# Performance work log

Measured on AMD Instinct MI355X. Metric: run time of the kernel, lower is better.

The kernel has to match this reference:

```python
import jax, jax.numpy as jnp
import numpy as np

D_MODEL = 384; NHEAD = 8; HEAD_DIM = D_MODEL // NHEAD
NPTS = 4; LENC = 6; LDEC = 6; DFFN = 1536
BS = 2; SD = 12; SH = 12; SW = 12; NQ = 300
S = SD * SH * SW
_SCALE = 0.02
MSDA_KEYS = ('off_w', 'off_b', 'aw_w', 'aw_b', 'vp_w', 'vp_b', 'op_w', 'op_b')


def _ln(x, g, b, eps=1e-5):
    m = x.mean(-1, keepdims=True)
    v = ((x - m) ** 2).mean(-1, keepdims=True)
    return (x - m) / jnp.sqrt(v + eps) * g + b


def _lin(x, w, b):
    return x @ w.T + b


def _trilinear(val, loc):
    # val [B,C,D,H,W]; loc [B,Q,3] normalized (x,y,z) in [0,1].
    # align_corners=False grid_sample semantics, zero padding outside.
    B, C, Dd, Hh, Ww = val.shape
    x = loc[..., 0] * Ww - 0.5
    y = loc[..., 1] * Hh - 0.5
    z = loc[..., 2] * Dd - 0.5
    x0, y0, z0 = jnp.floor(x), jnp.floor(y), jnp.floor(z)
    fx, fy, fz = x - x0, y - y0, z - z0
    bidx = jnp.arange(B)[:, None]
    out = jnp.zeros((B, loc.shape[1], C), val.dtype)
    for dz in (0, 1):
        zi = z0 + dz
        wz = fz if dz else 1.0 - fz
        for dy in (0, 1):
            yi = y0 + dy
            wy = fy if dy else 1.0 - fy
            for dx in (0, 1):
                xi = x0 + dx
                wx = fx if dx else 1.0 - fx
                inb = (xi >= 0) & (xi < Ww) & (yi >= 0) & (yi < Hh) & (zi >= 0) & (zi < Dd)
                v = val[bidx, :,
                        jnp.clip(zi, 0, Dd - 1).astype(jnp.int32),
                        jnp.clip(yi, 0, Hh - 1).astype(jnp.int32),
                        jnp.clip(xi, 0, Ww - 1).astype(jnp.int32)]  # [B,Q,C]
                out = out + (wz * wy * wx * inb)[..., None] * v
    return out


def _msda(query, ref, src, pad_mask, p):
    # 3D multi-scale deformable attention, single feature level.
    B, Lq, _ = query.shape
    value = _lin(src, p['vp_w'], p['vp_b'])
    value = jnp.where(pad_mask[..., None], 0.0, value).reshape(B, S, NHEAD, HEAD_DIM)
    off = _lin(query, p['off_w'], p['off_b']).reshape(B, Lq, NHEAD, NPTS, 3)
    aw = jax.nn.softmax(_lin(query, p['aw_w'], p['aw_b']).reshape(B, Lq, NHEAD, NPTS), -1)
    norm = jnp.array([SW, SH, SD], jnp.float32)  # (x,y,z) normalizer
    loc = ref[:, :, None, None, :] + off / norm  # [B,Lq,H,P,3]
    val = value.transpose(0, 2, 3, 1).reshape(B * NHEAD, HEAD_DIM, SD, SH, SW)
    locf = loc.transpose(0, 2, 1, 3, 4).reshape(B * NHEAD, Lq * NPTS, 3)
    samp = _trilinear(val, locf).reshape(B, NHEAD, Lq, NPTS, HEAD_DIM)
    out = jnp.einsum('bqhp,bhqpc->bqhc', aw, samp).reshape(B, Lq, D_MODEL)
    return _lin(out, p['op_w'], p['op_b'])


def _mha(q, k, v, in_w, in_b, out_w, out_b):
    B, L, d = q.shape
    qp = _lin(q, in_w[:d], in_b[:d]).reshape(B, L, NHEAD, HEAD_DIM)
    kp = _lin(k, in_w[d:2 * d], in_b[d:2 * d]).reshape(B, L, NHEAD, HEAD_DIM)
    vp = _lin(v, in_w[2 * d:], in_b[2 * d:]).reshape(B, L, NHEAD, HEAD_DIM)
    attn = jax.nn.softmax(jnp.einsum('bqhc,bkhc->bhqk', qp, kp) * (1.0 / float(np.sqrt(HEAD_DIM))), -1)
    o = jnp.einsum('bhqk,bkhc->bqhc', attn, vp).reshape(B, L, d)
    return _lin(o, out_w, out_b)


def _forward(a):
    src = a['srcs'].reshape(BS, D_MODEL, S).transpose(0, 2, 1)
    pos = a['pos_embeds'].reshape(BS, D_MODEL, S).transpose(0, 2, 1) + a['level_embed'][0]
    mask = a['masks'].reshape(BS, S)
    m = a['masks']
    valid = jnp.stack([(~m[:, 0, 0, :]).sum(1) / SW,
                       (~m[:, 0, :, 0]).sum(1) / SH,
                       (~m[:, :, 0, 0]).sum(1) / SD], -1).astype(jnp.float32)  # [B,3] (w,h,d)
    rz, ry, rx = jnp.meshgrid((jnp.arange(SD, dtype=jnp.float32) + 0.5) / SD,
                              (jnp.arange(SH, dtype=jnp.float32) + 0.5) / SH,
                              (jnp.arange(SW, dtype=jnp.float32) + 0.5) / SW, indexing='ij')
    enc_ref = jnp.stack([rx.ravel(), ry.ravel(), rz.ravel()], -1)[None] * valid[:, None]  # [B,S,3]
    x = src
    for l in range(LENC):
        p = {n: a['e_' + n][l] for n in MSDA_KEYS}
        x2 = _msda(x + pos, enc_ref, x, mask, p)
        x = _ln(x + x2, a['e_n1_g'][l], a['e_n1_b'][l])
        h = jax.nn.relu(_lin(x, a['e_l1_w'][l], a['e_l1_b'][l]))
        x = _ln(x + _lin(h, a['e_l2_w'][l], a['e_l2_b'][l]), a['e_n2_g'][l], a['e_n2_b'][l])
    memory = x
    qe = jnp.broadcast_to(a['query_embed'][None, :, :D_MODEL], (BS, NQ, D_MODEL))
    y = jnp.broadcast_to(a['query_embed'][None, :, D_MODEL:], (BS, NQ, D_MODEL))
    ref_pts = jax.nn.sigmoid(_lin(qe, a['ref_w'], a['ref_b']))  # [B,NQ,3]
    dec_ref = ref_pts * valid[:, None]  # reference_points * valid_ratios (single level)
    for l in range(LDEC):
        q = y + qe
        y2 = _mha(q, q, y, a['d_sa_in_w'][l], a['d_sa_in_b'][l], a['d_sa_out_w'][l], a['d_sa_out_b'][l])
        y = _ln(y + y2, a['d_n2_g'][l], a['d_n2_b'][l])
        p = {n: a['d_' + n][l] for n in MSDA_KEYS}
        y2 = _msda(y + qe, dec_ref, memory, mask, p)
        y = _ln(y + y2, a['d_n1_g'][l], a['d_n1_b'][l])
        h = jax.nn.relu(_lin(y, a['d_l1_w'][l], a['d_l1_b'][l]))
        y = _ln(y + _lin(h, a['d_l2_w'][l], a['d_l2_b'][l]), a['d_n3_g'][l], a['d_n3_b'][l])
    return y


def setup_inputs():
    ks = iter(jax.random.split(jax.random.key(0), 40))

    def w(*shape):
        return jax.random.normal(next(ks), shape, jnp.float32) * _SCALE

    z = lambda *s: jnp.zeros(s, jnp.float32)
    o = lambda *s: jnp.ones(s, jnp.float32)
    inp = {
        'srcs': jax.random.normal(next(ks), (BS, D_MODEL, SD, SH, SW), jnp.float32),
        'masks': jnp.zeros((BS, SD, SH, SW), bool),
        'query_embed': jax.random.normal(next(ks), (NQ, 2 * D_MODEL), jnp.float32),
        'pos_embeds': jax.random.normal(next(ks), (BS, D_MODEL, SD, SH, SW), jnp.float32),
        'level_embed': jax.random.normal(next(ks), (1, D_MODEL), jnp.float32),
        'ref_w': w(3, D_MODEL), 'ref_b': z(3),
    }
    for pre, L in (('e_', LENC), ('d_', LDEC)):
        inp[pre + 'off_w'] = w(L, NHEAD * NPTS * 3, D_MODEL); inp[pre + 'off_b'] = z(L, NHEAD * NPTS * 3)
        inp[pre + 'aw_w'] = w(L, NHEAD * NPTS, D_MODEL); inp[pre + 'aw_b'] = z(L, NHEAD * NPTS)
        inp[pre + 'vp_w'] = w(L, D_MODEL, D_MODEL); inp[pre + 'vp_b'] = z(L, D_MODEL)
        inp[pre + 'op_w'] = w(L, D_MODEL, D_MODEL); inp[pre + 'op_b'] = z(L, D_MODEL)
        inp[pre + 'n1_g'] = o(L, D_MODEL); inp[pre + 'n1_b'] = z(L, D_MODEL)
        inp[pre + 'l1_w'] = w(L, DFFN, D_MODEL); inp[pre + 'l1_b'] = z(L, DFFN)
        inp[pre + 'l2_w'] = w(L, D_MODEL, DFFN); inp[pre + 'l2_b'] = z(L, D_MODEL)
        inp[pre + 'n2_g'] = o(L, D_MODEL); inp[pre + 'n2_b'] = z(L, D_MODEL)
    inp['d_sa_in_w'] = w(LDEC, 3 * D_MODEL, D_MODEL); inp['d_sa_in_b'] = z(LDEC, 3 * D_MODEL)
    inp['d_sa_out_w'] = w(LDEC, D_MODEL, D_MODEL); inp['d_sa_out_b'] = z(LDEC, D_MODEL)
    inp['d_n3_g'] = o(LDEC, D_MODEL); inp['d_n3_b'] = z(LDEC, D_MODEL)
    return inp


def reference(srcs, masks, query_embed, pos_embeds, level_embed, ref_w, ref_b,
              e_off_w, e_off_b, e_aw_w, e_aw_b, e_vp_w, e_vp_b, e_op_w, e_op_b,
              e_n1_g, e_n1_b, e_l1_w, e_l1_b, e_l2_w, e_l2_b, e_n2_g, e_n2_b,
              d_off_w, d_off_b, d_aw_w, d_aw_b, d_vp_w, d_vp_b, d_op_w, d_op_b,
              d_n1_g, d_n1_b, d_sa_in_w, d_sa_in_b, d_sa_out_w, d_sa_out_b,
              d_n2_g, d_n2_b, d_l1_w, d_l1_b, d_l2_w, d_l2_b, d_n3_g, d_n3_b):
    return _forward(dict(locals()))
```

## Files before the change

kernel.cpp:

```cpp
#include <hip/hip_runtime.h>
#include <math.h>

#define BS_   2
#define S_    1728
#define C_    384
#define H_    8
#define HD_   48
#define DFFN_ 1536
#define NQ_   300
#define GD_   12

typedef __attribute__((ext_vector_type(8))) short short8;
typedef __attribute__((ext_vector_type(4))) float f32x4;

__device__ __forceinline__ ushort f2bf(float f) {
    union { float f; uint u; } v; v.f = f;
    uint u = v.u;
    uint r = (u + 0x7FFFu + ((u >> 16) & 1u)) >> 16;
    return (ushort)r;
}

__global__ __launch_bounds__(256) void f2bf_kernel(
    const float* __restrict__ src, ushort* __restrict__ dst, int n2)
{
    int i = blockIdx.x * 256 + threadIdx.x;
    if (i < n2) {
        float2 v = ((const float2*)src)[i];
        ushort2 o; o.x = f2bf(v.x); o.y = f2bf(v.y);
        ((ushort2*)dst)[i] = o;
    }
}

__global__ __launch_bounds__(256) void gemm_bf16_kernel(
    const ushort* __restrict__ A, const ushort* __restrict__ W,
    const float* __restrict__ bias, void* __restrict__ Co,
    int M, int N, int K, int flags)
{
    __shared__ __align__(16) ushort As[64][40];
    __shared__ __align__(16) ushort Ws[64][40];

    const int tid  = threadIdx.x;
    const int m0 = blockIdx.y * 64;
    const int n0 = blockIdx.x * 64;

    const int srow = tid >> 2;
    const int sch  = tid & 3;
    const int gmA  = m0 + srow;
    const int gnW  = n0 + srow;
    const size_t aBase = (size_t)gmA * K + sch * 8;
    const size_t wBase = (size_t)gnW * K + sch * 8;

    const int lane = tid & 63;
    const int w    = tid >> 6;
    const int wr   = (w >> 1) * 32;
    const int wc   = (w & 1) * 32;
    const int fr   = lane & 15;
    const int fks  = (lane >> 4) * 8;

    f32x4 acc[2][2] = {};

    short8 va = {}, vw = {};
    if (gmA < M) va = *(const short8*)(A + aBase);
    if (gnW < N) vw = *(const short8*)(W + wBase);

    for (int k0 = 0; k0 < K; k0 += 32) {
        *(short8*)&As[srow][sch * 8] = va;
        *(short8*)&Ws[srow][sch * 8] = vw;
        __syncthreads();
        if (k0 + 32 < K) {
            va = (gmA < M) ? *(const short8*)(A + aBase + k0 + 32) : short8{};
            vw = (gnW < N) ? *(const short8*)(W + wBase + k0 + 32) : short8{};
        }
        short8 af[2], bf[2];
        #pragma unroll
        for (int mi = 0; mi < 2; ++mi)
            af[mi] = *(const short8*)&As[wr + mi * 16 + fr][fks];
        #pragma unroll
        for (int ni = 0; ni < 2; ++ni)
            bf[ni] = *(const short8*)&Ws[wc + ni * 16 + fr][fks];
        #pragma unroll
        for (int mi = 0; mi < 2; ++mi)
            #pragma unroll
            for (int ni = 0; ni < 2; ++ni)
                acc[mi][ni] = __builtin_amdgcn_mfma_f32_16x16x32_bf16(
                    af[mi], bf[ni], acc[mi][ni], 0, 0, 0);
        __syncthreads();
    }

    const int r0 = (lane >> 4) * 4;
    const int relu = flags & 1;
    const int obf  = flags & 2;
    float* Cf = (float*)Co;
    ushort* Ch = (ushort*)Co;
    #pragma unroll
    for (int mi = 0; mi < 2; ++mi) {
        #pragma unroll
        for (int ni = 0; ni < 2; ++ni) {
            int gn = n0 + wc + ni * 16 + fr;
            if (gn >= N) continue;
            float bv = bias[gn];
            #pragma unroll
            for (int j = 0; j < 4; ++j) {
                int gm = m0 + wr + mi * 16 + r0 + j;
                if (gm >= M) continue;
                float v = acc[mi][ni][j] + bv;
                if (relu) v = fmaxf(v, 0.f);
                if (obf) Ch[(size_t)gm * N + gn] = f2bf(v);
                else     Cf[(size_t)gm * N + gn] = v;
            }
        }
    }
}

__global__ __launch_bounds__(64) void ln_kernel(
    const float* __restrict__ res, const float* __restrict__ delta,
    const float* __restrict__ g, const float* __restrict__ b,
    float* __restrict__ out, ushort* __restrict__ out_bf)
{
    const int row  = blockIdx.x;
    const int lane = threadIdx.x;
    const float* r = res   + (size_t)row * C_;
    const float* d = delta + (size_t)row * C_;
    float vals[6];
    float s = 0.f;
    #pragma unroll
    for (int i = 0; i < 6; ++i) {
        int c = lane + 64 * i;
        vals[i] = r[c] + d[c];
        s += vals[i];
    }
    #pragma unroll
    for (int off = 32; off; off >>= 1) s += __shfl_xor(s, off);
    float mean = s * (1.f / C_);
    float vs = 0.f;
    #pragma unroll
    for (int i = 0; i < 6; ++i) { float t = vals[i] - mean; vs += t * t; }
    #pragma unroll
    for (int off = 32; off; off >>= 1) vs += __shfl_xor(vs, off);
    float rstd = rsqrtf(vs * (1.f / C_) + 1e-5f);
    float* o = out + (size_t)row * C_;
    ushort* ob = out_bf + (size_t)row * C_;
    #pragma unroll
    for (int i = 0; i < 6; ++i) {
        int c = lane + 64 * i;
        float v = (vals[i] - mean) * rstd * g[c] + b[c];
        o[c] = v;
        ob[c] = f2bf(v);
    }
}

__global__ __launch_bounds__(384) void msda_kernel(
    const float* __restrict__ value,
    const float* __restrict__ offr,
    const float* __restrict__ awr,
    const float* __restrict__ ref,
    ushort* __restrict__ out,
    int Lq)
{
    const int bq = blockIdx.x;
    const int b = bq / Lq, q = bq % Lq;
    const int t = threadIdx.x;
    const int h = t / HD_, c = t % HD_;

    const float* aw = awr + ((size_t)(b * Lq + q)) * 32 + h * 4;
    float a0 = aw[0], a1 = aw[1], a2 = aw[2], a3 = aw[3];
    float mx = fmaxf(fmaxf(a0, a1), fmaxf(a2, a3));
    float e0 = __expf(a0 - mx), e1 = __expf(a1 - mx), e2 = __expf(a2 - mx), e3 = __expf(a3 - mx);
    float inv = 1.f / (e0 + e1 + e2 + e3);
    float wgt[4] = { e0 * inv, e1 * inv, e2 * inv, e3 * inv };

    const float* off = offr + ((size_t)(b * Lq + q)) * 96 + h * 12;
    float rx = ref[q * 3 + 0], ry = ref[q * 3 + 1], rz = ref[q * 3 + 2];
    const float* vb = value + (size_t)b * S_ * C_ + h * HD_ + c;

    float acc = 0.f;
    #pragma unroll
    for (int p = 0; p < 4; ++p) {
        float x = (rx + off[p * 3 + 0] * (1.f / GD_)) * GD_ - 0.5f;
        float y = (ry + off[p * 3 + 1] * (1.f / GD_)) * GD_ - 0.5f;
        float z = (rz + off[p * 3 + 2] * (1.f / GD_)) * GD_ - 0.5f;
        float x0f = floorf(x), y0f = floorf(y), z0f = floorf(z);
        float fx = x - x0f, fy = y - y0f, fz = z - z0f;
        int x0 = (int)x0f, y0 = (int)y0f, z0 = (int)z0f;
        float pv = 0.f;
        #pragma unroll
        for (int dz = 0; dz < 2; ++dz) {
            int zi = z0 + dz;
            if (zi < 0 || zi >= GD_) continue;
            float wz = dz ? fz : 1.f - fz;
            #pragma unroll
            for (int dy = 0; dy < 2; ++dy) {
                int yi = y0 + dy;
                if (yi < 0 || yi >= GD_) continue;
                float wy = dy ? fy : 1.f - fy;
                #pragma unroll
                for (int dx = 0; dx < 2; ++dx) {
                    int xi = x0 + dx;
                    if (xi < 0 || xi >= GD_) continue;
                    float wx = dx ? fx : 1.f - fx;
                    int s = (zi * GD_ + yi) * GD_ + xi;
                    pv += wz * wy * wx * vb[(size_t)s * C_];
                }
            }
        }
        acc += wgt[p] * pv;
    }
    out[((size_t)(b * Lq + q)) * C_ + t] = f2bf(acc);
}

__global__ __launch_bounds__(256) void attn_scores_kernel(
    const float* __restrict__ qp, const float* __restrict__ kp, float* __restrict__ sc)
{
    int idx = blockIdx.x * 256 + threadIdx.x;
    const int total = BS_ * H_ * NQ_ * NQ_;
    if (idx >= total) return;
    int j = idx % NQ_; int r = idx / NQ_;
    int i = r % NQ_;   r /= NQ_;
    int h = r % H_;    int b = r / H_;
    const float* qv = qp + ((size_t)(b * NQ_ + i)) * C_ + h * HD_;
    const float* kv = kp + ((size_t)(b * NQ_ + j)) * C_ + h * HD_;
    float s = 0.f;
    #pragma unroll
    for (int c = 0; c < HD_; ++c) s = fmaf(qv[c], kv[c], s);
    sc[idx] = s * 0.14433756729740643f;
}

__global__ __launch_bounds__(64) void softmax300_kernel(float* __restrict__ sc)
{
    const int row = blockIdx.x;
    float* p = sc + (size_t)row * NQ_;
    const int lane = threadIdx.x;
    float v[5];
    float mx = -INFINITY;
    #pragma unroll
    for (int i = 0; i < 5; ++i) {
        int c = lane + 64 * i;
        v[i] = (c < NQ_) ? p[c] : -INFINITY;
        mx = fmaxf(mx, v[i]);
    }
    #pragma unroll
    for (int off = 32; off; off >>= 1) mx = fmaxf(mx, __shfl_xor(mx, off));
    float s = 0.f;
    #pragma unroll
    for (int i = 0; i < 5; ++i) {
        int c = lane + 64 * i;
        v[i] = (c < NQ_) ? __expf(v[i] - mx) : 0.f;
        s += v[i];
    }
    #pragma unroll
    for (int off = 32; off; off >>= 1) s += __shfl_xor(s, off);
    float inv = 1.f / s;
    #pragma unroll
    for (int i = 0; i < 5; ++i) {
        int c = lane + 64 * i;
        if (c < NQ_) p[c] = v[i] * inv;
    }
}

__global__ __launch_bounds__(256) void attn_out_kernel(
    const float* __restrict__ sc, const float* __restrict__ vp, ushort* __restrict__ o)
{
    int idx = blockIdx.x * 256 + threadIdx.x;
    const int total = BS_ * NQ_ * C_;
    if (idx >= total) return;
    int c = idx % C_; int r = idx / C_;
    int i = r % NQ_;  int b = r / NQ_;
    int h = c / HD_;
    const float* srow = sc + (((size_t)(b * H_ + h)) * NQ_ + i) * NQ_;
    const float* v = vp + (size_t)b * NQ_ * C_ + c;
    float acc = 0.f;
    for (int j = 0; j < NQ_; ++j) acc = fmaf(srow[j], v[(size_t)j * C_], acc);
    o[idx] = f2bf(acc);
}

__global__ __launch_bounds__(256) void prep_kernel(
    const float* __restrict__ srcs, const float* __restrict__ posin,
    const float* __restrict__ lvl, float* __restrict__ x, ushort* __restrict__ x_bf,
    float* __restrict__ pos)
{
    int idx = blockIdx.x * 256 + threadIdx.x;
    const int total = BS_ * S_ * C_;
    if (idx >= total) return;
    int c = idx % C_; int r = idx / C_;
    int s = r % S_;   int b = r / S_;
    size_t si = ((size_t)b * C_ + c) * S_ + s;
    float xv = srcs[si];
    x[idx]   = xv;
    x_bf[idx] = f2bf(xv);
    pos[idx] = posin[si] + lvl[c];
}

__global__ __launch_bounds__(64) void encref_kernel(float* __restrict__ eref)
{
    int s = blockIdx.x * 64 + threadIdx.x;
    if (s >= S_) return;
    int w = s % GD_, h = (s / GD_) % GD_, d = s / (GD_ * GD_);
    eref[s * 3 + 0] = (w + 0.5f) / GD_;
    eref[s * 3 + 1] = (h + 0.5f) / GD_;
    eref[s * 3 + 2] = (d + 0.5f) / GD_;
}

__global__ __launch_bounds__(64) void decref_kernel(
    const float* __restrict__ qemb, const float* __restrict__ rw,
    const float* __restrict__ rb, float* __restrict__ dref)
{
    int idx = blockIdx.x * 64 + threadIdx.x;
    if (idx >= NQ_ * 3) return;
    int d = idx % 3, q = idx / 3;
    const float* qe = qemb + (size_t)q * 768;
    const float* w = rw + d * C_;
    float s = rb[d];
    for (int c = 0; c < C_; ++c) s = fmaf(qe[c], w[c], s);
    dref[idx] = 1.f / (1.f + __expf(-s));
}

__global__ __launch_bounds__(256) void add_bf_kernel(
    const float* __restrict__ a, const float* __restrict__ b, ushort* __restrict__ o, int n)
{
    int idx = blockIdx.x * 256 + threadIdx.x;
    if (idx < n) o[idx] = f2bf(a[idx] + b[idx]);
}

__global__ __launch_bounds__(256) void add_qe_kernel(
    const float* __restrict__ y, const float* __restrict__ qemb, ushort* __restrict__ o)
{
    int idx = blockIdx.x * 256 + threadIdx.x;
    const int total = BS_ * NQ_ * C_;
    if (idx >= total) return;
    int c = idx % C_; int q = (idx / C_) % NQ_;
    o[idx] = f2bf(y[idx] + qemb[(size_t)q * 768 + c]);
}

__global__ __launch_bounds__(256) void init_y_kernel(
    const float* __restrict__ qemb, float* __restrict__ y, ushort* __restrict__ y_bf)
{
    int idx = blockIdx.x * 256 + threadIdx.x;
    const int total = BS_ * NQ_ * C_;
    if (idx >= total) return;
    int c = idx % C_; int q = (idx / C_) % NQ_;
    float v = qemb[(size_t)q * 768 + 384 + c];
    y[idx] = v;
    y_bf[idx] = f2bf(v);
}

static inline void gemm(const ushort* A, const ushort* W, const float* bias, void* C,
                        int M, int N, int K, int flags, hipStream_t s)
{
    dim3 g((N + 63) / 64, (M + 63) / 64);
    hipLaunchKernelGGL(gemm_bf16_kernel, g, dim3(256), 0, s, A, W, bias, C, M, N, K, flags);
}

static inline void conv_w(const float* src, ushort* dst, size_t n, hipStream_t s)
{
    int n2 = (int)(n / 2);
    hipLaunchKernelGGL(f2bf_kernel, dim3((n2 + 255) / 256), dim3(256), 0, s, src, dst, n2);
}

extern "C" void kernel_launch(void* const* d_in, const int* in_sizes, int n_in,
                              void* d_out, int out_size, void* d_ws, size_t ws_size,
                              hipStream_t stream)
{
    const float* srcs    = (const float*)d_in[0];
    const float* qemb    = (const float*)d_in[2];
    const float* posin   = (const float*)d_in[3];
    const float* lvl     = (const float*)d_in[4];
    const float* ref_w   = (const float*)d_in[5];
    const float* ref_b   = (const float*)d_in[6];
    const float* e_off_w = (const float*)d_in[7];
    const float* e_off_b = (const float*)d_in[8];
    const float* e_aw_w  = (const float*)d_in[9];
    const float* e_aw_b  = (const float*)d_in[10];
    const float* e_vp_w  = (const float*)d_in[11];
    const float* e_vp_b  = (const float*)d_in[12];
    const float* e_op_w  = (const float*)d_in[13];
    const float* e_op_b  = (const float*)d_in[14];
    const float* e_n1_g  = (const float*)d_in[15];
    const float* e_n1_b  = (const float*)d_in[16];
    const float* e_l1_w  = (const float*)d_in[17];
    const float* e_l1_b  = (const float*)d_in[18];
    const float* e_l2_w  = (const float*)d_in[19];
    const float* e_l2_b  = (const float*)d_in[20];
    const float* e_n2_g  = (const float*)d_in[21];
    const float* e_n2_b  = (const float*)d_in[22];
    const float* dd_off_w = (const float*)d_in[23];
    const float* dd_off_b = (const float*)d_in[24];
    const float* dd_aw_w  = (const float*)d_in[25];
    const float* dd_aw_b  = (const float*)d_in[26];
    const float* dd_vp_w  = (const float*)d_in[27];
    const float* dd_vp_b  = (const float*)d_in[28];
    const float* dd_op_w  = (const float*)d_in[29];
    const float* dd_op_b  = (const float*)d_in[30];
    const float* dd_n1_g  = (const float*)d_in[31];
    const float* dd_n1_b  = (const float*)d_in[32];
    const float* dd_l1_w  = (const float*)d_in[33];
    const float* dd_l1_b  = (const float*)d_in[34];
    const float* dd_l2_w  = (const float*)d_in[35];
    const float* dd_l2_b  = (const float*)d_in[36];
    const float* dd_n2_g  = (const float*)d_in[37];
    const float* dd_n2_b  = (const float*)d_in[38];
    const float* sa_in_w  = (const float*)d_in[39];
    const float* sa_in_b  = (const float*)d_in[40];
    const float* sa_out_w = (const float*)d_in[41];
    const float* sa_out_b = (const float*)d_in[42];
    const float* dd_n3_g  = (const float*)d_in[43];
    const float* dd_n3_b  = (const float*)d_in[44];

    float* ws = (float*)d_ws;
    size_t o = 0;
    const size_t NXC = (size_t)BS_ * S_ * C_;
    const size_t NYC = (size_t)BS_ * NQ_ * C_;
    float* x     = ws + o; o += NXC;
    float* pos   = ws + o; o += NXC;
    float* value = ws + o; o += NXC;
    float* x2    = ws + o; o += NXC;
    float* offb  = ws + o; o += (size_t)BS_ * S_ * 96;
    float* awb   = ws + o; o += (size_t)BS_ * S_ * 32;
    float* eref  = ws + o; o += (size_t)S_ * 3 + 64;
    float* dref  = ws + o; o += (size_t)NQ_ * 3 + 64;
    float* y     = ws + o; o += NYC;
    float* qp    = ws + o; o += NYC;
    float* kp    = ws + o; o += NYC;
    float* vpb   = ws + o; o += NYC;
    float* sc    = ws + o; o += (size_t)BS_ * H_ * NQ_ * NQ_;
    o = (o + 7) & ~(size_t)7;

    ushort* bws = (ushort*)(ws + o);
    size_t ob = 0;
    ushort* x_bf    = bws + ob; ob += NXC;
    ushort* qb_bf   = bws + ob; ob += NXC;
    ushort* samp_bf = bws + ob; ob += NXC;
    ushort* hbuf_bf = bws + ob; ob += (size_t)BS_ * S_ * DFFN_;
    ushort* y_bf    = bws + ob; ob += NYC;
    const size_t SZ_OFF = (size_t)6 * 96 * C_;
    const size_t SZ_AW  = (size_t)6 * 32 * C_;
    const size_t SZ_SQ  = (size_t)6 * C_ * C_;
    const size_t SZ_L1  = (size_t)6 * DFFN_ * C_;
    ushort* wb_e_off = bws + ob; ob += SZ_OFF;
    ushort* wb_e_aw  = bws + ob; ob += SZ_AW;
    ushort* wb_e_vp  = bws + ob; ob += SZ_SQ;
    ushort* wb_e_op  = bws + ob; ob += SZ_SQ;
    ushort* wb_e_l1  = bws + ob; ob += SZ_L1;
    ushort* wb_e_l2  = bws + ob; ob += SZ_L1;
    ushort* wb_d_off = bws + ob; ob += SZ_OFF;
    ushort* wb_d_aw  = bws + ob; ob += SZ_AW;
    ushort* wb_d_vp  = bws + ob; ob += SZ_SQ;
    ushort* wb_d_op  = bws + ob; ob += SZ_SQ;
    ushort* wb_d_l1  = bws + ob; ob += SZ_L1;
    ushort* wb_d_l2  = bws + ob; ob += SZ_L1;
    ushort* wb_sa_in = bws + ob; ob += (size_t)6 * 3 * C_ * C_;
    ushort* wb_sa_out= bws + ob; ob += SZ_SQ;

    conv_w(e_off_w, wb_e_off, SZ_OFF, stream);
    conv_w(e_aw_w,  wb_e_aw,  SZ_AW,  stream);
    conv_w(e_vp_w,  wb_e_vp,  SZ_SQ,  stream);
    conv_w(e_op_w,  wb_e_op,  SZ_SQ,  stream);
    conv_w(e_l1_w,  wb_e_l1,  SZ_L1,  stream);
    conv_w(e_l2_w,  wb_e_l2,  SZ_L1,  stream);
    conv_w(dd_off_w, wb_d_off, SZ_OFF, stream);
    conv_w(dd_aw_w,  wb_d_aw,  SZ_AW,  stream);
    conv_w(dd_vp_w,  wb_d_vp,  SZ_SQ,  stream);
    conv_w(dd_op_w,  wb_d_op,  SZ_SQ,  stream);
    conv_w(dd_l1_w,  wb_d_l1,  SZ_L1,  stream);
    conv_w(dd_l2_w,  wb_d_l2,  SZ_L1,  stream);
    conv_w(sa_in_w,  wb_sa_in, (size_t)6 * 3 * C_ * C_, stream);
    conv_w(sa_out_w, wb_sa_out, SZ_SQ, stream);

    const int nEnc = BS_ * S_ * C_;
    const int nDec = BS_ * NQ_ * C_;
    const int encBlocks = (nEnc + 255) / 256;
    const int decBlocks = (nDec + 255) / 256;

    hipLaunchKernelGGL(prep_kernel, dim3(encBlocks), dim3(256), 0, stream, srcs, posin, lvl, x, x_bf, pos);
    hipLaunchKernelGGL(encref_kernel, dim3((S_ + 63) / 64), dim3(64), 0, stream, eref);

    for (int l = 0; l < 6; ++l) {
        hipLaunchKernelGGL(add_bf_kernel, dim3(encBlocks), dim3(256), 0, stream, x, pos, qb_bf, nEnc);
        gemm(x_bf, wb_e_vp + (size_t)l * C_ * C_, e_vp_b + (size_t)l * C_, value, BS_ * S_, C_, C_, 0, stream);
        gemm(qb_bf, wb_e_off + (size_t)l * 96 * C_, e_off_b + (size_t)l * 96, offb, BS_ * S_, 96, C_, 0, stream);
        gemm(qb_bf, wb_e_aw + (size_t)l * 32 * C_, e_aw_b + (size_t)l * 32, awb, BS_ * S_, 32, C_, 0, stream);
        hipLaunchKernelGGL(msda_kernel, dim3(BS_ * S_), dim3(384), 0, stream,
                           value, offb, awb, eref, samp_bf, S_);
        gemm(samp_bf, wb_e_op + (size_t)l * C_ * C_, e_op_b + (size_t)l * C_, x2, BS_ * S_, C_, C_, 0, stream);
        hipLaunchKernelGGL(ln_kernel, dim3(BS_ * S_), dim3(64), 0, stream,
                           x, x2, e_n1_g + (size_t)l * C_, e_n1_b + (size_t)l * C_, x, x_bf);
        gemm(x_bf, wb_e_l1 + (size_t)l * DFFN_ * C_, e_l1_b + (size_t)l * DFFN_, hbuf_bf,
             BS_ * S_, DFFN_, C_, 1 | 2, stream);
        gemm(hbuf_bf, wb_e_l2 + (size_t)l * C_ * DFFN_, e_l2_b + (size_t)l * C_, x2,
             BS_ * S_, C_, DFFN_, 0, stream);
        hipLaunchKernelGGL(ln_kernel, dim3(BS_ * S_), dim3(64), 0, stream,
                           x, x2, e_n2_g + (size_t)l * C_, e_n2_b + (size_t)l * C_, x, x_bf);
    }

    hipLaunchKernelGGL(init_y_kernel, dim3(decBlocks), dim3(256), 0, stream, qemb, y, y_bf);
    hipLaunchKernelGGL(decref_kernel, dim3((NQ_ * 3 + 63) / 64), dim3(64), 0, stream,
                       qemb, ref_w, ref_b, dref);

    const int scTotal = BS_ * H_ * NQ_ * NQ_;
    for (int l = 0; l < 6; ++l) {
        const ushort* inw = wb_sa_in + (size_t)l * 3 * C_ * C_;
        const float*  inb = sa_in_b + (size_t)l * 3 * C_;

        hipLaunchKernelGGL(add_qe_kernel, dim3(decBlocks), dim3(256), 0, stream, y, qemb, qb_bf);
        gemm(qb_bf, inw,                       inb,          qp,  BS_ * NQ_, C_, C_, 0, stream);
        gemm(qb_bf, inw + (size_t)C_ * C_,     inb + C_,     kp,  BS_ * NQ_, C_, C_, 0, stream);
        gemm(y_bf,  inw + (size_t)2 * C_ * C_, inb + 2 * C_, vpb, BS_ * NQ_, C_, C_, 0, stream);
        hipLaunchKernelGGL(attn_scores_kernel, dim3((scTotal + 255) / 256), dim3(256), 0, stream,
                           qp, kp, sc);
        hipLaunchKernelGGL(softmax300_kernel, dim3(BS_ * H_ * NQ_), dim3(64), 0, stream, sc);
        hipLaunchKernelGGL(attn_out_kernel, dim3(decBlocks), dim3(256), 0, stream, sc, vpb, samp_bf);
        gemm(samp_bf, wb_sa_out + (size_t)l * C_ * C_, sa_out_b + (size_t)l * C_, x2,
             BS_ * NQ_, C_, C_, 0, stream);
        hipLaunchKernelGGL(ln_kernel, dim3(BS_ * NQ_), dim3(64), 0, stream,
                           y, x2, dd_n2_g + (size_t)l * C_, dd_n2_b + (size_t)l * C_, y, y_bf);

        hipLaunchKernelGGL(add_qe_kernel, dim3(decBlocks), dim3(256), 0, stream, y, qemb, qb_bf);
        gemm(x_bf, wb_d_vp + (size_t)l * C_ * C_, dd_vp_b + (size_t)l * C_, value,
             BS_ * S_, C_, C_, 0, stream);
        gemm(qb_bf, wb_d_off + (size_t)l * 96 * C_, dd_off_b + (size_t)l * 96, offb,
             BS_ * NQ_, 96, C_, 0, stream);
        gemm(qb_bf, wb_d_aw + (size_t)l * 32 * C_, dd_aw_b + (size_t)l * 32, awb,
             BS_ * NQ_, 32, C_, 0, stream);
        hipLaunchKernelGGL(msda_kernel, dim3(BS_ * NQ_), dim3(384), 0, stream,
                           value, offb, awb, dref, samp_bf, NQ_);
        gemm(samp_bf, wb_d_op + (size_t)l * C_ * C_, dd_op_b + (size_t)l * C_, x2,
             BS_ * NQ_, C_, C_, 0, stream);
        hipLaunchKernelGGL(ln_kernel, dim3(BS_ * NQ_), dim3(64), 0, stream,
                           y, x2, dd_n1_g + (size_t)l * C_, dd_n1_b + (size_t)l * C_, y, y_bf);

        gemm(y_bf, wb_d_l1 + (size_t)l * DFFN_ * C_, dd_l1_b + (size_t)l * DFFN_, hbuf_bf,
             BS_ * NQ_, DFFN_, C_, 1 | 2, stream);
        gemm(hbuf_bf, wb_d_l2 + (size_t)l * C_ * DFFN_, dd_l2_b + (size_t)l * C_, x2,
             BS_ * NQ_, C_, DFFN_, 0, stream);
        float* lnout = (l == 5) ? (float*)d_out : y;
        hipLaunchKernelGGL(ln_kernel, dim3(BS_ * NQ_), dim3(64), 0, stream,
                           y, x2, dd_n3_g + (size_t)l * C_, dd_n3_b + (size_t)l * C_, lnout, y_bf);
    }
}
```

Before: 2.332 ms.

## Fuse self-attention into MFMA kernel, batch weight conversion, widen GEMM tiles

Replaces the three-kernel decoder self-attention (scores, softmax, output) with one fused MFMA flash-style kernel that keeps K/V in swizzled LDS. Weight conversion is batched into a single table-driven kernel. Offset and attention-weight projections are merged into one GEMM, with the query+pos add folded into the GEMM A-load, and Q/K projections are merged. The value projection is stored as bf16 for the MSDA gather, and the GEMM tile grows to 128x64. This cuts launch count and memory traffic at the cost of lower value precision and fewer blocks for small-M GEMMs.

```diff
diff --git a/kernel.cpp b/kernel.cpp
--- a/kernel.cpp
+++ b/kernel.cpp
@@ -19,91 +19,155 @@
     uint r = (u + 0x7FFFu + ((u >> 16) & 1u)) >> 16;
     return (ushort)r;
 }
-
-__global__ __launch_bounds__(256) void f2bf_kernel(
-    const float* __restrict__ src, ushort* __restrict__ dst, int n2)
+__device__ __forceinline__ float bf2f(ushort h) {
+    union { uint u; float f; } v; v.u = ((uint)h) << 16;
+    return v.f;
+}
+
+#define CT_N 34
+struct ConvTab {
+    const float* src[CT_N];
+    ushort* dst[CT_N];
+    int n[CT_N];
+    int cum[CT_N + 1];
+};
+__global__ __launch_bounds__(256) void convall_kernel(ConvTab t)
+{
+    int blk = blockIdx.x;
+    int e = 0;
+    while (blk >= t.cum[e + 1]) ++e;
+    int local = blk - t.cum[e];
+    int base = local * 2048 + (int)threadIdx.x * 8;
+    if (base >= t.n[e]) return;
+    const float* s = t.src[e] + base;
+    float4 a = *(const float4*)s;
+    float4 b = *(const float4*)(s + 4);
+    short8 o;
+    o[0] = (short)f2bf(a.x); o[1] = (short)f2bf(a.y);
+    o[2] = (short)f2bf(a.z); o[3] = (short)f2bf(a.w);
+    o[4] = (short)f2bf(b.x); o[5] = (short)f2bf(b.y);
+    o[6] = (short)f2bf(b.z); o[7] = (short)f2bf(b.w);
+    *(short8*)(t.dst[e] + base) = o;
+}
+
+__global__ __launch_bounds__(256) void biaspack_kernel(
+    const float* __restrict__ eoff, const float* __restrict__ eaw,
+    const float* __restrict__ doff, const float* __restrict__ daw,
+    float* __restrict__ be, float* __restrict__ bd)
 {
     int i = blockIdx.x * 256 + threadIdx.x;
-    if (i < n2) {
-        float2 v = ((const float2*)src)[i];
-        ushort2 o; o.x = f2bf(v.x); o.y = f2bf(v.y);
-        ((ushort2*)dst)[i] = o;
-    }
-}
-
-__global__ __launch_bounds__(256) void gemm_bf16_kernel(
-    const ushort* __restrict__ A, const ushort* __restrict__ W,
-    const float* __restrict__ bias, void* __restrict__ Co,
-    int M, int N, int K, int flags)
-{
-    __shared__ __align__(16) ushort As[64][40];
+    if (i >= 768) return;
+    int l = i >> 7, p = i & 127;
+    be[i] = (p < 96) ? eoff[l * 96 + p] : eaw[l * 32 + p - 96];
+    bd[i] = (p < 96) ? doff[l * 96 + p] : daw[l * 32 + p - 96];
+}
+
+template<int AMODE>
+__global__ __launch_bounds__(256) void gemm128_kernel(
+    const void* __restrict__ Aptr, const float* __restrict__ A1,
+    int lda1, int rowmod,
+    const ushort* __restrict__ W, const float* __restrict__ bias,
+    void* __restrict__ Co, int M, int N, int K, int flags)
+{
+    __shared__ __align__(16) ushort As[128][40];
     __shared__ __align__(16) ushort Ws[64][40];
 
-    const int tid  = threadIdx.x;
-    const int m0 = blockIdx.y * 64;
+    const int tid = threadIdx.x;
+    const int m0 = blockIdx.y * 128;
     const int n0 = blockIdx.x * 64;
 
-    const int srow = tid >> 2;
-    const int sch  = tid & 3;
-    const int gmA  = m0 + srow;
-    const int gnW  = n0 + srow;
-    const size_t aBase = (size_t)gmA * K + sch * 8;
-    const size_t wBase = (size_t)gnW * K + sch * 8;
+    const int arow = tid >> 1;
+    const int acol = (tid & 1) * 16;
+    const int gmA = m0 + arow;
+    const int wrow = tid >> 2;
+    const int wcol = (tid & 3) * 8;
+    const int gnW = n0 + wrow;
 
     const int lane = tid & 63;
-    const int w    = tid >> 6;
-    const int wr   = (w >> 1) * 32;
-    const int wc   = (w & 1) * 32;
-    const int fr   = lane & 15;
-    const int fks  = (lane >> 4) * 8;
-
-    f32x4 acc[2][2] = {};
-
-    short8 va = {}, vw = {};
-    if (gmA < M) va = *(const short8*)(A + aBase);
-    if (gnW < N) vw = *(const short8*)(W + wBase);
+    const int w = tid >> 6;
+    const int wm = (w >> 1) * 64;
+    const int wn = (w & 1) * 32;
+    const int fr = lane & 15;
+    const int fq = lane >> 4;
+
+    const ushort* Ab = (const ushort*)Aptr;
+    const float* a0f = (const float*)Aptr;
+    int a1row = 0;
+    if (AMODE == 1 && gmA < M) a1row = gmA % rowmod;
+
+    f32x4 acc[4][2] = {};
+
+    short8 va[2] = {}, vw = {};
+    if (gmA < M) {
+        if (AMODE == 0) {
+            va[0] = *(const short8*)(Ab + (size_t)gmA * K + acol);
+            va[1] = *(const short8*)(Ab + (size_t)gmA * K + acol + 8);
+        } else {
+            const float* p0 = a0f + (size_t)gmA * K + acol;
+            const float* p1 = A1 + (size_t)a1row * lda1 + acol;
+            #pragma unroll
+            for (int c = 0; c < 2; ++c)
+                #pragma unroll
+                for (int j = 0; j < 8; ++j)
+                    va[c][j] = (short)f2bf(p0[c * 8 + j] + p1[c * 8 + j]);
+        }
+    }
+    if (gnW < N) vw = *(const short8*)(W + (size_t)gnW * K + wcol);
 
     for (int k0 = 0; k0 < K; k0 += 32) {
-        *(short8*)&As[srow][sch * 8] = va;
-        *(short8*)&Ws[srow][sch * 8] = vw;
+        *(short8*)&As[arow][acol] = va[0];
+        *(short8*)&As[arow][acol + 8] = va[1];
+        *(short8*)&Ws[wrow][wcol] = vw;
         __syncthreads();
         if (k0 + 32 < K) {
-            va = (gmA < M) ? *(const short8*)(A + aBase + k0 + 32) : short8{};
-            vw = (gnW < N) ? *(const short8*)(W + wBase + k0 + 32) : short8{};
-        }
-        short8 af[2], bf[2];
-        #pragma unroll
-        for (int mi = 0; mi < 2; ++mi)
-            af[mi] = *(const short8*)&As[wr + mi * 16 + fr][fks];
+            if (gmA < M) {
+                if (AMODE == 0) {
+                    va[0] = *(const short8*)(Ab + (size_t)gmA * K + k0 + 32 + acol);
+                    va[1] = *(const short8*)(Ab + (size_t)gmA * K + k0 + 32 + acol + 8);
+                } else {
+                    const float* p0 = a0f + (size_t)gmA * K + k0 + 32 + acol;
+                    const float* p1 = A1 + (size_t)a1row * lda1 + k0 + 32 + acol;
+                    #pragma unroll
+                    for (int c = 0; c < 2; ++c)
+                        #pragma unroll
+                        for (int j = 0; j < 8; ++j)
+                            va[c][j] = (short)f2bf(p0[c * 8 + j] + p1[c * 8 + j]);
+                }
+            }
+            if (gnW < N) vw = *(const short8*)(W + (size_t)gnW * K + k0 + 32 + wcol);
+        }
+        short8 af[4], bw[2];
+        #pragma unroll
+        for (int fi = 0; fi < 4; ++fi)
+            af[fi] = *(const short8*)&As[wm + fi * 16 + fr][fq * 8];
         #pragma unroll
         for (int ni = 0; ni < 2; ++ni)
-            bf[ni] = *(const short8*)&Ws[wc + ni * 16 + fr][fks];
-        #pragma unroll
-        for (int mi = 0; mi < 2; ++mi)
+            bw[ni] = *(const short8*)&Ws[wn + ni * 16 + fr][fq * 8];
+        #pragma unroll
+        for (int fi = 0; fi < 4; ++fi)
             #pragma unroll
             for (int ni = 0; ni < 2; ++ni)
-                acc[mi][ni] = __builtin_amdgcn_mfma_f32_16x16x32_bf16(
-                    af[mi], bf[ni], acc[mi][ni], 0, 0, 0);
+                acc[fi][ni] = __builtin_amdgcn_mfma_f32_16x16x32_bf16(
+                    af[fi], bw[ni], acc[fi][ni], 0, 0, 0);
         __syncthreads();
     }
 
-    const int r0 = (lane >> 4) * 4;
     const int relu = flags & 1;
-    const int obf  = flags & 2;
+    const int obf = flags & 2;
     float* Cf = (float*)Co;
     ushort* Ch = (ushort*)Co;
     #pragma unroll
-    for (int mi = 0; mi < 2; ++mi) {
+    for (int fi = 0; fi < 4; ++fi) {
         #pragma unroll
         for (int ni = 0; ni < 2; ++ni) {
-            int gn = n0 + wc + ni * 16 + fr;
+            int gn = n0 + wn + ni * 16 + fr;
             if (gn >= N) continue;
             float bv = bias[gn];
             #pragma unroll
             for (int j = 0; j < 4; ++j) {
-                int gm = m0 + wr + mi * 16 + r0 + j;
+                int gm = m0 + wm + fi * 16 + fq * 4 + j;
                 if (gm >= M) continue;
-                float v = acc[mi][ni][j] + bv;
+                float v = acc[fi][ni][j] + bv;
                 if (relu) v = fmaxf(v, 0.f);
                 if (obf) Ch[(size_t)gm * N + gn] = f2bf(v);
                 else     Cf[(size_t)gm * N + gn] = v;
@@ -112,14 +176,141 @@
     }
 }
 
+__global__ __launch_bounds__(256) void mha_fused_kernel(
+    const float* __restrict__ qk, const float* __restrict__ vpb,
+    ushort* __restrict__ out)
+{
+    __shared__ __align__(16) ushort kv[20480];
+    __shared__ __align__(16) ushort pbuf[4][640];
+
+    const int qt = blockIdx.x;
+    const int bh = blockIdx.y;
+    const int b = bh >> 3, h = bh & 7;
+    const int tid = threadIdx.x;
+    const int lane = tid & 63, wv = tid >> 6;
+    const int fr = lane & 15, fq = lane >> 4;
+
+    const float* kbase = qk + (size_t)b * 300 * 768 + 384 + h * 48;
+    for (int idx = tid; idx < 320 * 64; idx += 256) {
+        int key = idx >> 6, d = idx & 63;
+        int byte = (key * 128 + d * 2) ^ ((key & 7) << 4);
+        ushort v = 0;
+        if (key < 300 && d < 48) v = f2bf(kbase[(size_t)key * 768 + d]);
+        *(ushort*)((char*)kv + byte) = v;
+    }
+
+    int q = qt * 64 + wv * 16 + fr;
+    short8 aq[2] = {short8{}, short8{}};
+    if (q < 300) {
+        const float* qrow = qk + ((size_t)(b * 300 + q)) * 768 + h * 48;
+        #pragma unroll
+        for (int half = 0; half < 2; ++half)
+            #pragma unroll
+            for (int j = 0; j < 8; ++j) {
+                int d = half * 32 + fq * 8 + j;
+                if (d < 48) aq[half][j] = (short)f2bf(qrow[d]);
+            }
+    }
+    __syncthreads();
+
+    f32x4 sfr[20];
+    #pragma unroll
+    for (int t = 0; t < 20; ++t) {
+        int key = t * 16 + fr;
+        short8 bk[2];
+        #pragma unroll
+        for (int half = 0; half < 2; ++half) {
+            int byte = (key * 128 + (half * 32 + fq * 8) * 2) ^ ((key & 7) << 4);
+            bk[half] = *(const short8*)((const char*)kv + byte);
+        }
+        f32x4 c = {};
+        c = __builtin_amdgcn_mfma_f32_16x16x32_bf16(aq[0], bk[0], c, 0, 0, 0);
+        c = __builtin_amdgcn_mfma_f32_16x16x32_bf16(aq[1], bk[1], c, 0, 0, 0);
+        sfr[t] = c;
+    }
+    if (fr >= 12) { sfr[18][0] = sfr[18][1] = sfr[18][2] = sfr[18][3] = -1e30f; }
+    sfr[19][0] = sfr[19][1] = sfr[19][2] = sfr[19][3] = -1e30f;
+
+    const float scale = 0.14433756729740643f;
+    float m[4], l[4];
+    #pragma unroll
+    for (int j = 0; j < 4; ++j) {
+        float mm = -1e30f;
+        #pragma unroll
+        for (int t = 0; t < 20; ++t) mm = fmaxf(mm, sfr[t][j]);
+        #pragma unroll
+        for (int msk = 1; msk < 16; msk <<= 1) mm = fmaxf(mm, __shfl_xor(mm, msk));
+        m[j] = mm;
+    }
+    #pragma unroll
+    for (int j = 0; j < 4; ++j) {
+        float ss = 0.f;
+        #pragma unroll
+        for (int t = 0; t < 20; ++t) {
+            float p = __expf((sfr[t][j] - m[j]) * scale);
+            sfr[t][j] = p;
+            ss += p;
+        }
+        #pragma unroll
+        for (int msk = 1; msk < 16; msk <<= 1) ss += __shfl_xor(ss, msk);
+        l[j] = ss;
+    }
+
+    __syncthreads();
+    const float* vbase = vpb + (size_t)b * 300 * 384 + h * 48;
+    for (int idx = tid; idx < 48 * 320; idx += 256) {
+        int d = idx / 320, key = idx - d * 320;
+        int byte = (d * 640 + key * 2) ^ ((d & 7) << 4);
+        ushort v = 0;
+        if (key < 300) v = f2bf(vbase[(size_t)key * 384 + d]);
+        *(ushort*)((char*)kv + byte) = v;
+    }
+    __syncthreads();
+
+    f32x4 o0 = {}, o1 = {}, o2 = {};
+    ushort* pw = &pbuf[wv][0];
+    for (int ch = 0; ch < 10; ++ch) {
+        #pragma unroll
+        for (int tt = 0; tt < 2; ++tt) {
+            int t = 2 * ch + tt;
+            #pragma unroll
+            for (int j = 0; j < 4; ++j)
+                pw[(fq * 4 + j) * 40 + tt * 16 + fr] = f2bf(sfr[t][j]);
+        }
+        asm volatile("s_waitcnt lgkmcnt(0)" ::: "memory");
+        short8 pa = *(const short8*)&pw[fr * 40 + fq * 8];
+        short8 bv[3];
+        #pragma unroll
+        for (int dt = 0; dt < 3; ++dt) {
+            int d = dt * 16 + fr;
+            int byte = (d * 640 + (ch * 32 + fq * 8) * 2) ^ ((d & 7) << 4);
+            bv[dt] = *(const short8*)((const char*)kv + byte);
+        }
+        o0 = __builtin_amdgcn_mfma_f32_16x16x32_bf16(pa, bv[0], o0, 0, 0, 0);
+        o1 = __builtin_amdgcn_mfma_f32_16x16x32_bf16(pa, bv[1], o1, 0, 0, 0);
+        o2 = __builtin_amdgcn_mfma_f32_16x16x32_bf16(pa, bv[2], o2, 0, 0, 0);
+    }
+
+    #pragma unroll
+    for (int j = 0; j < 4; ++j) {
+        int qq = qt * 64 + wv * 16 + fq * 4 + j;
+        if (qq >= 300) continue;
+        float invl = 1.f / l[j];
+        ushort* orow = out + ((size_t)(b * 300 + qq)) * 384 + h * 48;
+        orow[fr]      = f2bf(o0[j] * invl);
+        orow[16 + fr] = f2bf(o1[j] * invl);
+        orow[32 + fr] = f2bf(o2[j] * invl);
+    }
+}
+
 __global__ __launch_bounds__(64) void ln_kernel(
     const float* __restrict__ res, const float* __restrict__ delta,
     const float* __restrict__ g, const float* __restrict__ b,
     float* __restrict__ out, ushort* __restrict__ out_bf)
 {
-    const int row  = blockIdx.x;
+    const int row = blockIdx.x;
     const int lane = threadIdx.x;
-    const float* r = res   + (size_t)row * C_;
+    const float* r = res + (size_t)row * C_;
     const float* d = delta + (size_t)row * C_;
     float vals[6];
     float s = 0.f;
@@ -150,28 +341,28 @@
 }
 
 __global__ __launch_bounds__(384) void msda_kernel(
-    const float* __restrict__ value,
-    const float* __restrict__ offr,
-    const float* __restrict__ awr,
+    const ushort* __restrict__ value,
+    const float* __restrict__ offaw,
     const float* __restrict__ ref,
     ushort* __restrict__ out,
     int Lq)
 {
     const int bq = blockIdx.x;
-    const int b = bq / Lq, q = bq % Lq;
+    const int b = bq / Lq, qi = bq % Lq;
     const int t = threadIdx.x;
     const int h = t / HD_, c = t % HD_;
 
-    const float* aw = awr + ((size_t)(b * Lq + q)) * 32 + h * 4;
+    const float* row = offaw + ((size_t)(b * Lq + qi)) * 128;
+    const float* aw = row + 96 + h * 4;
     float a0 = aw[0], a1 = aw[1], a2 = aw[2], a3 = aw[3];
     float mx = fmaxf(fmaxf(a0, a1), fmaxf(a2, a3));
     float e0 = __expf(a0 - mx), e1 = __expf(a1 - mx), e2 = __expf(a2 - mx), e3 = __expf(a3 - mx);
     float inv = 1.f / (e0 + e1 + e2 + e3);
     float wgt[4] = { e0 * inv, e1 * inv, e2 * inv, e3 * inv };
 
-    const float* off = offr + ((size_t)(b * Lq + q)) * 96 + h * 12;
-    float rx = ref[q * 3 + 0], ry = ref[q * 3 + 1], rz = ref[q * 3 + 2];
-    const float* vb = value + (size_t)b * S_ * C_ + h * HD_ + c;
+    const float* off = row + h * 12;
+    float rx = ref[qi * 3 + 0], ry = ref[qi * 3 + 1], rz = ref[qi * 3 + 2];
+    const ushort* vb = value + (size_t)b * S_ * C_ + h * HD_ + c;
 
     float acc = 0.f;
     #pragma unroll
@@ -199,78 +390,13 @@
                     if (xi < 0 || xi >= GD_) continue;
                     float wx = dx ? fx : 1.f - fx;
                     int s = (zi * GD_ + yi) * GD_ + xi;
-                    pv += wz * wy * wx * vb[(size_t)s * C_];
+                    pv += wz * wy * wx * bf2f(vb[(size_t)s * C_]);
                 }
             }
         }
         acc += wgt[p] * pv;
     }
-    out[((size_t)(b * Lq + q)) * C_ + t] = f2bf(acc);
-}
-
-__global__ __launch_bounds__(256) void attn_scores_kernel(
-    const float* __restrict__ qp, const float* __restrict__ kp, float* __restrict__ sc)
-{
-    int idx = blockIdx.x * 256 + threadIdx.x;
-    const int total = BS_ * H_ * NQ_ * NQ_;
-    if (idx >= total) return;
-    int j = idx % NQ_; int r = idx / NQ_;
-    int i = r % NQ_;   r /= NQ_;
-    int h = r % H_;    int b = r / H_;
-    const float* qv = qp + ((size_t)(b * NQ_ + i)) * C_ + h * HD_;
-    const float* kv = kp + ((size_t)(b * NQ_ + j)) * C_ + h * HD_;
-    float s = 0.f;
-    #pragma unroll
-    for (int c = 0; c < HD_; ++c) s = fmaf(qv[c], kv[c], s);
-    sc[idx] = s * 0.14433756729740643f;
-}
-
-__global__ __launch_bounds__(64) void softmax300_kernel(float* __restrict__ sc)
-{
-    const int row = blockIdx.x;
-    float* p = sc + (size_t)row * NQ_;
-    const int lane = threadIdx.x;
-    float v[5];
-    float mx = -INFINITY;
-    #pragma unroll
-    for (int i = 0; i < 5; ++i) {
-        int c = lane + 64 * i;
-        v[i] = (c < NQ_) ? p[c] : -INFINITY;
-        mx = fmaxf(mx, v[i]);
-    }
-    #pragma unroll
-    for (int off = 32; off; off >>= 1) mx = fmaxf(mx, __shfl_xor(mx, off));
-    float s = 0.f;
-    #pragma unroll
-    for (int i = 0; i < 5; ++i) {
-        int c = lane + 64 * i;
-        v[i] = (c < NQ_) ? __expf(v[i] - mx) : 0.f;
-        s += v[i];
-    }
-    #pragma unroll
-    for (int off = 32; off; off >>= 1) s += __shfl_xor(s, off);
-    float inv = 1.f / s;
-    #pragma unroll
-    for (int i = 0; i < 5; ++i) {
-        int c = lane + 64 * i;
-        if (c < NQ_) p[c] = v[i] * inv;
-    }
-}
-
-__global__ __launch_bounds__(256) void attn_out_kernel(
-    const float* __restrict__ sc, const float* __restrict__ vp, ushort* __restrict__ o)
-{
-    int idx = blockIdx.x * 256 + threadIdx.x;
-    const int total = BS_ * NQ_ * C_;
-    if (idx >= total) return;
-    int c = idx % C_; int r = idx / C_;
-    int i = r % NQ_;  int b = r / NQ_;
-    int h = c / HD_;
-    const float* srow = sc + (((size_t)(b * H_ + h)) * NQ_ + i) * NQ_;
-    const float* v = vp + (size_t)b * NQ_ * C_ + c;
-    float acc = 0.f;
-    for (int j = 0; j < NQ_; ++j) acc = fmaf(srow[j], v[(size_t)j * C_], acc);
-    o[idx] = f2bf(acc);
+    out[((size_t)(b * Lq + qi)) * C_ + t] = f2bf(acc);
 }
 
 __global__ __launch_bounds__(256) void prep_kernel(
@@ -285,7 +411,7 @@
     int s = r % S_;   int b = r / S_;
     size_t si = ((size_t)b * C_ + c) * S_ + s;
     float xv = srcs[si];
-    x[idx]   = xv;
+    x[idx] = xv;
     x_bf[idx] = f2bf(xv);
     pos[idx] = posin[si] + lvl[c];
 }
@@ -314,23 +440,6 @@
     dref[idx] = 1.f / (1.f + __expf(-s));
 }
 
-__global__ __launch_bounds__(256) void add_bf_kernel(
-    const float* __restrict__ a, const float* __restrict__ b, ushort* __restrict__ o, int n)
-{
-    int idx = blockIdx.x * 256 + threadIdx.x;
-    if (idx < n) o[idx] = f2bf(a[idx] + b[idx]);
-}
-
-__global__ __launch_bounds__(256) void add_qe_kernel(
-    const float* __restrict__ y, const float* __restrict__ qemb, ushort* __restrict__ o)
-{
-    int idx = blockIdx.x * 256 + threadIdx.x;
-    const int total = BS_ * NQ_ * C_;
-    if (idx >= total) return;
-    int c = idx % C_; int q = (idx / C_) % NQ_;
-    o[idx] = f2bf(y[idx] + qemb[(size_t)q * 768 + c]);
-}
-
 __global__ __launch_bounds__(256) void init_y_kernel(
     const float* __restrict__ qemb, float* __restrict__ y, ushort* __restrict__ y_bf)
 {
@@ -343,17 +452,20 @@
     y_bf[idx] = f2bf(v);
 }
 
-static inline void gemm(const ushort* A, const ushort* W, const float* bias, void* C,
-                        int M, int N, int K, int flags, hipStream_t s)
-{
-    dim3 g((N + 63) / 64, (M + 63) / 64);
-    hipLaunchKernelGGL(gemm_bf16_kernel, g, dim3(256), 0, s, A, W, bias, C, M, N, K, flags);
-}
-
-static inline void conv_w(const float* src, ushort* dst, size_t n, hipStream_t s)
-{
-    int n2 = (int)(n / 2);
-    hipLaunchKernelGGL(f2bf_kernel, dim3((n2 + 255) / 256), dim3(256), 0, s, src, dst, n2);
+static inline void gemm0(const ushort* A, const ushort* W, const float* bias, void* C,
+                         int M, int N, int K, int flags, hipStream_t s)
+{
+    dim3 g((N + 63) / 64, (M + 127) / 128);
+    hipLaunchKernelGGL(gemm128_kernel<0>, g, dim3(256), 0, s,
+                       (const void*)A, (const float*)nullptr, 0, 1, W, bias, C, M, N, K, flags);
+}
+static inline void gemm1(const float* A0, const float* A1, int lda1, int rowmod,
+                         const ushort* W, const float* bias, void* C,
+                         int M, int N, int K, int flags, hipStream_t s)
+{
+    dim3 g((N + 63) / 64, (M + 127) / 128);
+    hipLaunchKernelGGL(gemm128_kernel<1>, g, dim3(256), 0, s,
+                       (const void*)A0, A1, lda1, rowmod, W, bias, C, M, N, K, flags);
 }
 
 extern "C" void kernel_launch(void* const* d_in, const int* in_sizes, int n_in,
@@ -398,10 +510,10 @@
     const float* dd_l2_b  = (const float*)d_in[36];
     const float* dd_n2_g  = (const float*)d_in[37];
     const float* dd_n2_b  = (const float*)d_in[38];
-    const float* sa_in_w  = (const float*)d_in[39];
-    const float* sa_in_b  = (const float*)d_in[40];
-    const float* sa_out_w = (const float*)d_in[41];
-    const float* sa_out_b = (const float*)d_in[42];
+    const float* dd_sa_in_w  = (const float*)d_in[39];
+    const float* dd_sa_in_b  = (const float*)d_in[40];
+    const float* dd_sa_out_w = (const float*)d_in[41];
+    const float* dd_sa_out_b = (const float*)d_in[42];
     const float* dd_n3_g  = (const float*)d_in[43];
     const float* dd_n3_b  = (const float*)d_in[44];
 
@@ -409,84 +521,90 @@
     size_t o = 0;
     const size_t NXC = (size_t)BS_ * S_ * C_;
     const size_t NYC = (size_t)BS_ * NQ_ * C_;
-    float* x     = ws + o; o += NXC;
-    float* pos   = ws + o; o += NXC;
-    float* value = ws + o; o += NXC;
-    float* x2    = ws + o; o += NXC;
-    float* offb  = ws + o; o += (size_t)BS_ * S_ * 96;
-    float* awb   = ws + o; o += (size_t)BS_ * S_ * 32;
-    float* eref  = ws + o; o += (size_t)S_ * 3 + 64;
-    float* dref  = ws + o; o += (size_t)NQ_ * 3 + 64;
-    float* y     = ws + o; o += NYC;
-    float* qp    = ws + o; o += NYC;
-    float* kp    = ws + o; o += NYC;
-    float* vpb   = ws + o; o += NYC;
-    float* sc    = ws + o; o += (size_t)BS_ * H_ * NQ_ * NQ_;
+    float* x      = ws + o; o += NXC;
+    float* pos    = ws + o; o += NXC;
+    float* x2     = ws + o; o += NXC;
+    float* offawE = ws + o; o += (size_t)BS_ * S_ * 128;
+    float* qk     = ws + o; o += (size_t)BS_ * NQ_ * 768;
+    float* vpb    = ws + o; o += NYC;
+    float* y      = ws + o; o += NYC;
+    float* eref   = ws + o; o += (size_t)S_ * 3 + 64;
+    float* dref   = ws + o; o += (size_t)NQ_ * 3 + 64;
+    float* offawBe = ws + o; o += 768;
+    float* offawBd = ws + o; o += 768;
     o = (o + 7) & ~(size_t)7;
 
     ushort* bws = (ushort*)(ws + o);
     size_t ob = 0;
     ushort* x_bf    = bws + ob; ob += NXC;
-    ushort* qb_bf   = bws + ob; ob += NXC;
     ushort* samp_bf = bws + ob; ob += NXC;
     ushort* hbuf_bf = bws + ob; ob += (size_t)BS_ * S_ * DFFN_;
     ushort* y_bf    = bws + ob; ob += NYC;
-    const size_t SZ_OFF = (size_t)6 * 96 * C_;
-    const size_t SZ_AW  = (size_t)6 * 32 * C_;
-    const size_t SZ_SQ  = (size_t)6 * C_ * C_;
-    const size_t SZ_L1  = (size_t)6 * DFFN_ * C_;
-    ushort* wb_e_off = bws + ob; ob += SZ_OFF;
-    ushort* wb_e_aw  = bws + ob; ob += SZ_AW;
-    ushort* wb_e_vp  = bws + ob; ob += SZ_SQ;
-    ushort* wb_e_op  = bws + ob; ob += SZ_SQ;
-    ushort* wb_e_l1  = bws + ob; ob += SZ_L1;
-    ushort* wb_e_l2  = bws + ob; ob += SZ_L1;
-    ushort* wb_d_off = bws + ob; ob += SZ_OFF;
-    ushort* wb_d_aw  = bws + ob; ob += SZ_AW;
-    ushort* wb_d_vp  = bws + ob; ob += SZ_SQ;
-    ushort* wb_d_op  = bws + ob; ob += SZ_SQ;
-    ushort* wb_d_l1  = bws + ob; ob += SZ_L1;
-    ushort* wb_d_l2  = bws + ob; ob += SZ_L1;
-    ushort* wb_sa_in = bws + ob; ob += (size_t)6 * 3 * C_ * C_;
-    ushort* wb_sa_out= bws + ob; ob += SZ_SQ;
-
-    conv_w(e_off_w, wb_e_off, SZ_OFF, stream);
-    conv_w(e_aw_w,  wb_e_aw,  SZ_AW,  stream);
-    conv_w(e_vp_w,  wb_e_vp,  SZ_SQ,  stream);
-    conv_w(e_op_w,  wb_e_op,  SZ_SQ,  stream);
-    conv_w(e_l1_w,  wb_e_l1,  SZ_L1,  stream);
-    conv_w(e_l2_w,  wb_e_l2,  SZ_L1,  stream);
-    conv_w(dd_off_w, wb_d_off, SZ_OFF, stream);
-    conv_w(dd_aw_w,  wb_d_aw,  SZ_AW,  stream);
-    conv_w(dd_vp_w,  wb_d_vp,  SZ_SQ,  stream);
-    conv_w(dd_op_w,  wb_d_op,  SZ_SQ,  stream);
-    conv_w(dd_l1_w,  wb_d_l1,  SZ_L1,  stream);
-    conv_w(dd_l2_w,  wb_d_l2,  SZ_L1,  stream);
-    conv_w(sa_in_w,  wb_sa_in, (size_t)6 * 3 * C_ * C_, stream);
-    conv_w(sa_out_w, wb_sa_out, SZ_SQ, stream);
+    ushort* value   = bws + ob; ob += NXC;
+    const size_t SZ_OFFAW = (size_t)6 * 128 * C_;
+    const size_t SZ_SQ    = (size_t)6 * C_ * C_;
+    const size_t SZ_L1    = (size_t)6 * DFFN_ * C_;
+    ushort* wOffawE = bws + ob; ob += SZ_OFFAW;
+    ushort* wOffawD = bws + ob; ob += SZ_OFFAW;
+    ushort* wVpE = bws + ob; ob += SZ_SQ;
+    ushort* wOpE = bws + ob; ob += SZ_SQ;
+    ushort* wL1E = bws + ob; ob += SZ_L1;
+    ushort* wL2E = bws + ob; ob += SZ_L1;
+    ushort* wVpD = bws + ob; ob += SZ_SQ;
+    ushort* wOpD = bws + ob; ob += SZ_SQ;
+    ushort* wL1D = bws + ob; ob += SZ_L1;
+    ushort* wL2D = bws + ob; ob += SZ_L1;
+    ushort* wSaIn = bws + ob; ob += (size_t)6 * 3 * C_ * C_;
+    ushort* wSaOut = bws + ob; ob += SZ_SQ;
+
+    ConvTab ct;
+    int ne = 0;
+    auto addent = [&](const float* s, ushort* d, int n) {
+        ct.src[ne] = s; ct.dst[ne] = d; ct.n[ne] = n; ++ne;
+    };
+    for (int l = 0; l < 6; ++l) addent(e_off_w + (size_t)l * 96 * C_, wOffawE + (size_t)l * 128 * C_, 96 * C_);
+    for (int l = 0; l < 6; ++l) addent(e_aw_w + (size_t)l * 32 * C_, wOffawE + (size_t)l * 128 * C_ + 96 * C_, 32 * C_);
+    for (int l = 0; l < 6; ++l) addent(dd_off_w + (size_t)l * 96 * C_, wOffawD + (size_t)l * 128 * C_, 96 * C_);
+    for (int l = 0; l < 6; ++l) addent(dd_aw_w + (size_t)l * 32 * C_, wOffawD + (size_t)l * 128 * C_ + 96 * C_, 32 * C_);
+    addent(e_vp_w, wVpE, (int)SZ_SQ);
+    addent(e_op_w, wOpE, (int)SZ_SQ);
+    addent(e_l1_w, wL1E, (int)SZ_L1);
+    addent(e_l2_w, wL2E, (int)SZ_L1);
+    addent(dd_vp_w, wVpD, (int)SZ_SQ);
+    addent(dd_op_w, wOpD, (int)SZ_SQ);
+    addent(dd_l1_w, wL1D, (int)SZ_L1);
+    addent(dd_l2_w, wL2D, (int)SZ_L1);
+    addent(dd_sa_in_w, wSaIn, (int)((size_t)6 * 3 * C_ * C_));
+    addent(dd_sa_out_w, wSaOut, (int)SZ_SQ);
+    ct.cum[0] = 0;
+    for (int e = 0; e < CT_N; ++e) ct.cum[e + 1] = ct.cum[e] + (ct.n[e] + 2047) / 2048;
+    hipLaunchKernelGGL(convall_kernel, dim3(ct.cum[CT_N]), dim3(256), 0, stream, ct);
+    hipLaunchKernelGGL(biaspack_kernel, dim3(3), dim3(256), 0, stream,
+                       e_off_b, e_aw_b, dd_off_b, dd_aw_b, offawBe, offawBd);
 
     const int nEnc = BS_ * S_ * C_;
+    const int encBlocks = (nEnc + 255) / 256;
     const int nDec = BS_ * NQ_ * C_;
-    const int encBlocks = (nEnc + 255) / 256;
     const int decBlocks = (nDec + 255) / 256;
 
     hipLaunchKernelGGL(prep_kernel, dim3(encBlocks), dim3(256), 0, stream, srcs, posin, lvl, x, x_bf, pos);
     hipLaunchKernelGGL(encref_kernel, dim3((S_ + 63) / 64), dim3(64), 0, stream, eref);
 
     for (int l = 0; l < 6; ++l) {
-        hipLaunchKernelGGL(add_bf_kernel, dim3(encBlocks), dim3(256), 0, stream, x, pos, qb_bf, nEnc);
-        gemm(x_bf, wb_e_vp + (size_t)l * C_ * C_, e_vp_b + (size_t)l * C_, value, BS_ * S_, C_, C_, 0, stream);
-        gemm(qb_bf, wb_e_off + (size_t)l * 96 * C_, e_off_b + (size_t)l * 96, offb, BS_ * S_, 96, C_, 0, stream);
-        gemm(qb_bf, wb_e_aw + (size_t)l * 32 * C_, e_aw_b + (size_t)l * 32, awb, BS_ * S_, 32, C_, 0, stream);
+        gemm0(x_bf, wVpE + (size_t)l * C_ * C_, e_vp_b + (size_t)l * C_, value,
+              BS_ * S_, C_, C_, 2, stream);
+        gemm1(x, pos, C_, BS_ * S_, wOffawE + (size_t)l * 128 * C_, offawBe + l * 128, offawE,
+              BS_ * S_, 128, C_, 0, stream);
         hipLaunchKernelGGL(msda_kernel, dim3(BS_ * S_), dim3(384), 0, stream,
-                           value, offb, awb, eref, samp_bf, S_);
-        gemm(samp_bf, wb_e_op + (size_t)l * C_ * C_, e_op_b + (size_t)l * C_, x2, BS_ * S_, C_, C_, 0, stream);
+                           value, offawE, eref, samp_bf, S_);
+        gemm0(samp_bf, wOpE + (size_t)l * C_ * C_, e_op_b + (size_t)l * C_, x2,
+              BS_ * S_, C_, C_, 0, stream);
         hipLaunchKernelGGL(ln_kernel, dim3(BS_ * S_), dim3(64), 0, stream,
                            x, x2, e_n1_g + (size_t)l * C_, e_n1_b + (size_t)l * C_, x, x_bf);
-        gemm(x_bf, wb_e_l1 + (size_t)l * DFFN_ * C_, e_l1_b + (size_t)l * DFFN_, hbuf_bf,
-             BS_ * S_, DFFN_, C_, 1 | 2, stream);
-        gemm(hbuf_bf, wb_e_l2 + (size_t)l * C_ * DFFN_, e_l2_b + (size_t)l * C_, x2,
-             BS_ * S_, C_, DFFN_, 0, stream);
+        gemm0(x_bf, wL1E + (size_t)l * DFFN_ * C_, e_l1_b + (size_t)l * DFFN_, hbuf_bf,
+              BS_ * S_, DFFN_, C_, 1 | 2, stream);
+        gemm0(hbuf_bf, wL2E + (size_t)l * C_ * DFFN_, e_l2_b + (size_t)l * C_, x2,
+              BS_ * S_, C_, DFFN_, 0, stream);
         hipLaunchKernelGGL(ln_kernel, dim3(BS_ * S_), dim3(64), 0, stream,
                            x, x2, e_n2_g + (size_t)l * C_, e_n2_b + (size_t)l * C_, x, x_bf);
     }
@@ -495,42 +613,33 @@
     hipLaunchKernelGGL(decref_kernel, dim3((NQ_ * 3 + 63) / 64), dim3(64), 0, stream,
                        qemb, ref_w, ref_b, dref);
 
-    const int scTotal = BS_ * H_ * NQ_ * NQ_;
     for (int l = 0; l < 6; ++l) {
-        const ushort* inw = wb_sa_in + (size_t)l * 3 * C_ * C_;
-        const float*  inb = sa_in_b + (size_t)l * 3 * C_;
-
-        hipLaunchKernelGGL(add_qe_kernel, dim3(decBlocks), dim3(256), 0, stream, y, qemb, qb_bf);
-        gemm(qb_bf, inw,                       inb,          qp,  BS_ * NQ_, C_, C_, 0, stream);
-        gemm(qb_bf, inw + (size_t)C_ * C_,     inb + C_,     kp,  BS_ * NQ_, C_, C_, 0, stream);
-        gemm(y_bf,  inw + (size_t)2 * C_ * C_, inb + 2 * C_, vpb, BS_ * NQ_, C_, C_, 0, stream);
-        hipLaunchKernelGGL(attn_scores_kernel, dim3((scTotal + 255) / 256), dim3(256), 0, stream,
-                           qp, kp, sc);
-        hipLaunchKernelGGL(softmax300_kernel, dim3(BS_ * H_ * NQ_), dim3(64), 0, stream, sc);
-        hipLaunchKernelGGL(attn_out_kernel, dim3(decBlocks), dim3(256), 0, stream, sc, vpb, samp_bf);
-        gemm(samp_bf, wb_sa_out + (size_t)l * C_ * C_, sa_out_b + (size_t)l * C_, x2,
-             BS_ * NQ_, C_, C_, 0, stream);
+        const ushort* inw = wSaIn + (size_t)l * 3 * C_ * C_;
+        const float* inb = dd_sa_in_b + (size_t)l * 3 * C_;
+
+        gemm1(y, qemb, 768, NQ_, inw, inb, qk, BS_ * NQ_, 768, C_, 0, stream);
+        gemm0(y_bf, inw + (size_t)2 * C_ * C_, inb + 2 * C_, vpb, BS_ * NQ_, C_, C_, 0, stream);
+        hipLaunchKernelGGL(mha_fused_kernel, dim3(5, 16), dim3(256), 0, stream, qk, vpb, samp_bf);
+        gemm0(samp_bf, wSaOut + (size_t)l * C_ * C_, dd_sa_out_b + (size_t)l * C_, x2,
+              BS_ * NQ_, C_, C_, 0, stream);
         hipLaunchKernelGGL(ln_kernel, dim3(BS_ * NQ_), dim3(64), 0, stream,
                            y, x2, dd_n2_g + (size_t)l * C_, dd_n2_b + (size_t)l * C_, y, y_bf);
 
-        hipLaunchKernelGGL(add_qe_kernel, dim3(decBlocks), dim3(256), 0, stream, y, qemb, qb_bf);
-        gemm(x_bf, wb_d_vp + (size_t)l * C_ * C_, dd_vp_b + (size_t)l * C_, value,
-             BS_ * S_, C_, C_, 0, stream);
-        gemm(qb_bf, wb_d_off + (size_t)l * 96 * C_, dd_off_b + (size_t)l * 96, offb,
-             BS_ * NQ_, 96, C_, 0, stream);
-        gemm(qb_bf, wb_d_aw + (size_t)l * 32 * C_, dd_aw_b + (size_t)l * 32, awb,
-             BS_ * NQ_, 32, C_, 0, stream);
+        gemm0(x_bf, wVpD + (size_t)l * C_ * C_, dd_vp_b + (size_t)l * C_, value,
+              BS_ * S_, C_, C_, 2, stream);
+        gemm1(y, qemb, 768, NQ_, wOffawD + (size_t)l * 128 * C_, offawBd + l * 128, offawE,
+              BS_ * NQ_, 128, C_, 0, stream);
         hipLaunchKernelGGL(msda_kernel, dim3(BS_ * NQ_), dim3(384), 0, stream,
-                           value, offb, awb, dref, samp_bf, NQ_);
-        gemm(samp_bf, wb_d_op + (size_t)l * C_ * C_, dd_op_b + (size_t)l * C_, x2,
-             BS_ * NQ_, C_, C_, 0, stream);
+                           value, offawE, dref, samp_bf, NQ_);
+        gemm0(samp_bf, wOpD + (size_t)l * C_ * C_, dd_op_b + (size_t)l * C_, x2,
+              BS_ * NQ_, C_, C_, 0, stream);
         hipLaunchKernelGGL(ln_kernel, dim3(BS_ * NQ_), dim3(64), 0, stream,
                            y, x2, dd_n1_g + (size_t)l * C_, dd_n1_b + (size_t)l * C_, y, y_bf);
 
-        gemm(y_bf, wb_d_l1 + (size_t)l * DFFN_ * C_, dd_l1_b + (size_t)l * DFFN_, hbuf_bf,
-             BS_ * NQ_, DFFN_, C_, 1 | 2, stream);
-        gemm(hbuf_bf, wb_d_l2 + (size_t)l * C_ * DFFN_, dd_l2_b + (size_t)l * C_, x2,
-             BS_ * NQ_, C_, DFFN_, 0, stream);
+        gemm0(y_bf, wL1D + (size_t)l * DFFN_ * C_, dd_l1_b + (size_t)l * DFFN_, hbuf_bf,
+              BS_ * NQ_, DFFN_, C_, 1 | 2, stream);
+        gemm0(hbuf_bf, wL2D + (size_t)l * C_ * DFFN_, dd_l2_b + (size_t)l * C_, x2,
+              BS_ * NQ_, C_, DFFN_, 0, stream);
         float* lnout = (l == 5) ? (float*)d_out : y;
         hipLaunchKernelGGL(ln_kernel, dim3(BS_ * NQ_), dim3(64), 0, stream,
                            y, x2, dd_n3_g + (size_t)l * C_, dd_n3_b + (size_t)l * C_, lnout, y_bf);
```

Result: slower. 2.379 ms (+2.0%).
